# Kernel optimization log

Hardware: AMD Instinct MI355X
Metric: run time of the kernel (lower is better)

Reference implementation:

```python
import jax, jax.numpy as jnp
import numpy as np

H = 4        # num_heads
D = 16       # d_hid (per-head dim)
INF = 1e9


def setup_inputs() -> dict:
    key = jax.random.key(0)
    ks = jax.random.split(key, 8)
    T, R, DT, DZ = 4, 384, 64, 128
    t = jax.random.normal(ks[0], (T, R, R, DT), dtype=jnp.float32)
    z = jax.random.normal(ks[1], (R, R, DZ), dtype=jnp.float32)
    template_mask = jnp.ones((T,), dtype=jnp.float32)
    wq = jax.random.normal(ks[2], (DZ, H * D), dtype=jnp.float32) * 0.08
    wk = jax.random.normal(ks[3], (DT, H * D), dtype=jnp.float32) * 0.12
    wv = jax.random.normal(ks[4], (DT, H * D), dtype=jnp.float32) * 0.12
    wo = jax.random.normal(ks[5], (H * D, DZ), dtype=jnp.float32) * 0.12
    bo = jnp.zeros((DZ,), dtype=jnp.float32)
    return {"t": t, "z": z, "template_mask": template_mask,
            "wq": wq, "wk": wk, "wv": wv, "wo": wo, "bo": bo}


def reference(t, z, template_mask, wq, wk, wv, wo, bo):
    # t: [T, R, R, d_t], z: [R, R, d_z], template_mask: [T]
    R = z.shape[0]
    scale = 1.0 / np.sqrt(float(D))
    # gen_attn_mask: 0 where mask > 0, -inf where masked out
    bias = jnp.where(template_mask > 0.0, 0.0, -INF)          # [T]
    # permute_final_dims(t, (1,2,0,3)): template axis becomes kv length
    tp = jnp.transpose(t, (1, 2, 0, 3))                        # [R, R, T, d_t]
    # q_len is 1 (z.unsqueeze(-2)); fold it away
    q = (z @ wq).reshape(R, R, H, D) * scale                   # [R, R, H, D]
    k = (tp @ wk).reshape(R, R, -1, H, D)                      # [R, R, T, H, D]
    v = (tp @ wv).reshape(R, R, -1, H, D)                      # [R, R, T, H, D]
    logits = jnp.einsum('xyhd,xythd->xyht', q, k) + bias       # [R, R, H, T]
    a = jax.nn.softmax(logits, axis=-1)
    o = jnp.einsum('xyht,xythd->xyhd', a, v).reshape(R, R, H * D)
    return o @ wo + bo                                         # [R, R, d_z]
```

## Files before the change

kernel.cpp:

```cpp
#include <hip/hip_runtime.h>


typedef __bf16 bf16x8 __attribute__((ext_vector_type(8)));
typedef float f32x4 __attribute__((ext_vector_type(4)));
typedef unsigned int u32x4 __attribute__((ext_vector_type(4)));
typedef unsigned int u32x2 __attribute__((ext_vector_type(2)));

#define MFMA16(A, B, C) __builtin_amdgcn_mfma_f32_16x16x32_bf16((A), (B), (C), 0, 0, 0)

#define BARRIER_LGKM()                                      \
  do {                                                      \
    asm volatile("s_waitcnt lgkmcnt(0)" ::: "memory");      \
    __builtin_amdgcn_sched_barrier(0);                      \
    __builtin_amdgcn_s_barrier();                           \
    __builtin_amdgcn_sched_barrier(0);                      \
    asm volatile("" ::: "memory");                          \
  } while (0)

__device__ __forceinline__ unsigned int cvtpk(float lo, float hi) {
  unsigned int r;
  asm("v_cvt_pk_bf16_f32 %0, %1, %2" : "=v"(r) : "v"(lo), "v"(hi));
  return r;
}

__device__ __forceinline__ bf16x8 pack8(float4 a, float4 b) {
  u32x4 u;
  u.x = cvtpk(a.x, a.y);
  u.y = cvtpk(a.z, a.w);
  u.z = cvtpk(b.x, b.y);
  u.w = cvtpk(b.z, b.w);
  return __builtin_bit_cast(bf16x8, u);
}

__device__ __forceinline__ bf16x8 ldsA(const char* smem, int baseByte, int row,
                                       int colElem, int strideElem) {
  int off = baseByte + (((row * strideElem + colElem) * 2) ^ ((row & 7) << 4));
  return __builtin_bit_cast(bf16x8, *(const u32x4*)(smem + off));
}

__device__ __forceinline__ bf16x8 ldsT(const char* TB, int tt, int px, int kElem) {
  int off = ((((tt * 64 + px) << 7) + (kElem << 1))) ^ ((px & 7) << 4);
  return __builtin_bit_cast(bf16x8, *(const u32x4*)(TB + off));
}

__device__ __forceinline__ void stage_w(char* smem, int off, float v, int r, int j) {
  unsigned int u = __float_as_uint(v);
  *(unsigned short*)(smem + off + ((j * 2) ^ ((r & 7) << 4))) =
      (unsigned short)((u + 0x7fffu + ((u >> 16) & 1u)) >> 16);
}

__global__ __launch_bounds__(256, 2)
void q_kernel(const float* __restrict__ z_, const float* __restrict__ wq_,
              u32x2* __restrict__ q_) {
  extern __shared__ char smem[];
  for (int i = threadIdx.x; i < 8192; i += 256) {
    int r = i >> 7, cc = i & 127;
    stage_w(smem, 0, wq_[cc * 64 + r] * 0.25f, r, i);
  }
  __syncthreads();
  const int lane = threadIdx.x & 63;
  const int wid = threadIdx.x >> 6;
  const int c = lane & 15, g = lane >> 4;
  const f32x4 vz = {0.f, 0.f, 0.f, 0.f};
  for (int tile = blockIdx.x * 4 + wid; tile < 9216; tile += 4608) {
    const int p = tile * 16 + c;
    const float4* zp = (const float4*)(z_ + (size_t)p * 128 + g * 8);
    float4 zraw[8];
#pragma unroll
    for (int s = 0; s < 4; ++s) {
      zraw[2 * s] = zp[s * 8];
      zraw[2 * s + 1] = zp[s * 8 + 1];
    }
    f32x4 qacc[4] = {vz, vz, vz, vz};
#pragma unroll
    for (int s = 0; s < 4; ++s) {
      bf16x8 zb = pack8(zraw[2 * s], zraw[2 * s + 1]);
#pragma unroll
      for (int h = 0; h < 4; ++h)
        qacc[h] = MFMA16(ldsA(smem, 0, h * 16 + c, s * 32 + g * 8, 128), zb, qacc[h]);
    }
#pragma unroll
    for (int h = 0; h < 4; ++h) {
      u32x2 w;
      w.x = cvtpk(qacc[h][0], qacc[h][1]);
      w.y = cvtpk(qacc[h][2], qacc[h][3]);
      q_[(size_t)(tile * 4 + h) * 64 + lane] = w;
    }
  }
}

__global__ __launch_bounds__(512, 1)
void tpa_b_kernel(const float* __restrict__ t_, const u32x2* __restrict__ q_,
                  const float* __restrict__ mask_,
                  const float* __restrict__ wk_, const float* __restrict__ wv_,
                  const float* __restrict__ wo_, const float* __restrict__ bo_,
                  float* __restrict__ out_) {
  extern __shared__ char smem[];
  char* TB = smem + 32768;

  for (int i = threadIdx.x; i < 16384; i += 512) {
    if (i < 4096) {
      int r = i >> 6, cc = i & 63;
      stage_w(smem, 0, wk_[cc * 64 + r], r, i);
    } else if (i < 8192) {
      int j = i - 4096, r = j >> 6, cc = j & 63;
      stage_w(smem, 8192, wv_[cc * 64 + r], r, j);
    } else {
      int j = i - 8192, r = j >> 6, cc = j & 63;
      stage_w(smem, 16384, wo_[cc * 128 + r], r, j);
    }
  }
  __syncthreads();

  const int tid = threadIdx.x;
  const int lane = tid & 63, wid = tid >> 6;
  const int c = lane & 15, g = lane >> 4;
  const int q4 = wid & 3;
  const int hp = wid >> 2;
  const int px = q4 * 16 + c;
  char* Olds = smem + 65536 + q4 * 2048;

  const float b0 = mask_[0] > 0.f ? 0.f : -1e9f;
  const float b1 = mask_[1] > 0.f ? 0.f : -1e9f;
  const float b2 = mask_[2] > 0.f ? 0.f : -1e9f;
  const float b3 = mask_[3] > 0.f ? 0.f : -1e9f;

  float4 bov[4];
#pragma unroll
  for (int m = 0; m < 4; ++m) bov[m] = *(const float4*)(bo_ + hp * 64 + m * 16 + g * 4);

  const int spx = tid >> 3;
  const int schunk = tid & 7;
  const f32x4 vz = {0.f, 0.f, 0.f, 0.f};

  float4 ra[8];
  u32x2 qcur[2], qnext[2];

  auto issue_step = [&](int step, u32x2* qw) {
    const float* base = t_ + ((size_t)step * 64 + spx) * 64 + schunk * 8;
#pragma unroll
    for (int tt = 0; tt < 4; ++tt) {
      const float* p4 = base + (size_t)tt * 9437184;
      ra[tt * 2] = *(const float4*)(p4);
      ra[tt * 2 + 1] = *(const float4*)(p4 + 4);
    }
    const int stile = step * 4 + q4;
#pragma unroll
    for (int h = 0; h < 2; ++h)
      qw[h] = q_[(size_t)(stile * 4 + hp * 2 + h) * 64 + lane];
  };

  issue_step(blockIdx.x, qcur);

  for (int k = 0; k < 9; ++k) {
    const int step = blockIdx.x + k * 256;

#pragma unroll
    for (int tt = 0; tt < 4; ++tt) {
      bf16x8 w = pack8(ra[tt * 2], ra[tt * 2 + 1]);
      int off = ((((tt * 64 + spx) << 7) + (schunk << 4))) ^ ((spx & 7) << 4);
      *(u32x4*)(TB + off) = __builtin_bit_cast(u32x4, w);
    }
    if (k < 8) issue_step(step + 256, qnext);
    BARRIER_LGKM();

    f32x4 qacc[2];
#pragma unroll
    for (int h = 0; h < 2; ++h) {
      qacc[h][0] = __uint_as_float(qcur[h].x << 16);
      qacc[h][1] = __uint_as_float(qcur[h].x & 0xffff0000u);
      qacc[h][2] = __uint_as_float(qcur[h].y << 16);
      qacc[h][3] = __uint_as_float(qcur[h].y & 0xffff0000u);
    }
    f32x4 oacc[2] = {vz, vz};
    float ssum[2] = {0.f, 0.f};
#pragma unroll
    for (int tt = 0; tt < 4; ++tt) {
      bf16x8 tb0 = ldsT(TB, tt, px, g * 8);
      bf16x8 tb1 = ldsT(TB, tt, px, 32 + g * 8);
      const float bt = (tt == 0) ? b0 : (tt == 1) ? b1 : (tt == 2) ? b2 : b3;
#pragma unroll
      for (int h = 0; h < 2; ++h) {
        const int row = (hp * 2 + h) * 16 + c;
        f32x4 kacc = MFMA16(ldsA(smem, 0, row, g * 8, 64), tb0, vz);
        kacc = MFMA16(ldsA(smem, 0, row, 32 + g * 8, 64), tb1, kacc);
        f32x4 vacc = MFMA16(ldsA(smem, 8192, row, g * 8, 64), tb0, vz);
        vacc = MFMA16(ldsA(smem, 8192, row, 32 + g * 8, 64), tb1, vacc);
        float d = qacc[h][0] * kacc[0] + qacc[h][1] * kacc[1] +
                  qacc[h][2] * kacc[2] + qacc[h][3] * kacc[3];
        d += __shfl_xor(d, 16);
        d += __shfl_xor(d, 32);
        float e = __expf(d + bt);
        ssum[h] += e;
        oacc[h] += e * vacc;
      }
    }

#pragma unroll
    for (int h = 0; h < 2; ++h) {
      float inv = 1.0f / ssum[h];
      f32x4 o = oacc[h] * inv;
      u32x2 w;
      w.x = cvtpk(o[0], o[1]);
      w.y = cvtpk(o[2], o[3]);
      int off = (c * 128 + (hp * 2 + h) * 32 + g * 8) ^ ((c & 7) << 4);
      *(u32x2*)(Olds + off) = w;
    }
    BARRIER_LGKM();

    f32x4 outacc[4] = {vz, vz, vz, vz};
#pragma unroll
    for (int s = 0; s < 2; ++s) {
      int off = (c * 128 + s * 64 + g * 16) ^ ((c & 7) << 4);
      bf16x8 ob = __builtin_bit_cast(bf16x8, *(const u32x4*)(Olds + off));
#pragma unroll
      for (int m = 0; m < 4; ++m)
        outacc[m] = MFMA16(ldsA(smem, 16384, hp * 64 + m * 16 + c, s * 32 + g * 8, 64),
                           ob, outacc[m]);
    }
    float* op = out_ + ((size_t)step * 64 + px) * 128 + hp * 64;
#pragma unroll
    for (int m = 0; m < 4; ++m) {
      float4 st;
      st.x = outacc[m][0] + bov[m].x;
      st.y = outacc[m][1] + bov[m].y;
      st.z = outacc[m][2] + bov[m].z;
      st.w = outacc[m][3] + bov[m].w;
      *(float4*)(op + m * 16 + g * 4) = st;
    }
    if (k < 8) {
      qcur[0] = qnext[0];
      qcur[1] = qnext[1];
    }
  }
}

__global__ __launch_bounds__(256, 2)
void tpa_fused(const float* __restrict__ t_, const float* __restrict__ z_,
               const float* __restrict__ mask_,
               const float* __restrict__ wq_, const float* __restrict__ wk_,
               const float* __restrict__ wv_, const float* __restrict__ wo_,
               const float* __restrict__ bo_, float* __restrict__ out_) {
  extern __shared__ char smem[];
  for (int i = threadIdx.x; i < 24576; i += 256) {
    if (i < 8192) {
      int r = i >> 7;
      stage_w(smem, 0, wq_[(i & 127) * 64 + r] * 0.25f, r, i);
    } else if (i < 12288) {
      int j = i - 8192, r = j >> 6;
      stage_w(smem, 16384, wk_[(j & 63) * 64 + r], r, j);
    } else if (i < 16384) {
      int j = i - 12288, r = j >> 6;
      stage_w(smem, 24576, wv_[(j & 63) * 64 + r], r, j);
    } else {
      int j = i - 16384, r = j >> 6;
      stage_w(smem, 32768, wo_[(j & 63) * 128 + r], r, j);
    }
  }
  __syncthreads();
  const int lane = threadIdx.x & 63;
  const int wid = threadIdx.x >> 6;
  const int c = lane & 15, g = lane >> 4;
  const float b0 = mask_[0] > 0.f ? 0.f : -1e9f;
  const float b1 = mask_[1] > 0.f ? 0.f : -1e9f;
  const float b2 = mask_[2] > 0.f ? 0.f : -1e9f;
  const float b3 = mask_[3] > 0.f ? 0.f : -1e9f;
  char* Olds = smem + 49152 + wid * 2048;
  const f32x4 vz = {0.f, 0.f, 0.f, 0.f};
  for (int tile = blockIdx.x * 4 + wid; tile < 9216; tile += 2048) {
    const int p = tile * 16 + c;
    const float4* zp = (const float4*)(z_ + (size_t)p * 128 + g * 8);
    const float* tp = t_ + (size_t)p * 64 + g * 8;
    f32x4 qacc[4] = {vz, vz, vz, vz};
#pragma unroll
    for (int s = 0; s < 4; ++s) {
      bf16x8 zb = pack8(zp[s * 8], zp[s * 8 + 1]);
#pragma unroll
      for (int h = 0; h < 4; ++h)
        qacc[h] = MFMA16(ldsA(smem, 0, h * 16 + c, s * 32 + g * 8, 128), zb, qacc[h]);
    }
    f32x4 oacc[4] = {vz, vz, vz, vz};
    float ssum[4] = {0.f, 0.f, 0.f, 0.f};
#pragma unroll
    for (int tt = 0; tt < 4; ++tt) {
      const float* tq = tp + (size_t)tt * 9437184;
      bf16x8 tb0 = pack8(*(const float4*)(tq), *(const float4*)(tq + 4));
      bf16x8 tb1 = pack8(*(const float4*)(tq + 32), *(const float4*)(tq + 36));
      f32x4 kacc[4], vacc[4];
#pragma unroll
      for (int h = 0; h < 4; ++h) {
        kacc[h] = MFMA16(ldsA(smem, 16384, h * 16 + c, g * 8, 64), tb0, vz);
        kacc[h] = MFMA16(ldsA(smem, 16384, h * 16 + c, 32 + g * 8, 64), tb1, kacc[h]);
        vacc[h] = MFMA16(ldsA(smem, 24576, h * 16 + c, g * 8, 64), tb0, vz);
        vacc[h] = MFMA16(ldsA(smem, 24576, h * 16 + c, 32 + g * 8, 64), tb1, vacc[h]);
      }
      const float bt = (tt == 0) ? b0 : (tt == 1) ? b1 : (tt == 2) ? b2 : b3;
#pragma unroll
      for (int h = 0; h < 4; ++h) {
        float d = qacc[h][0] * kacc[h][0] + qacc[h][1] * kacc[h][1] +
                  qacc[h][2] * kacc[h][2] + qacc[h][3] * kacc[h][3];
        d += __shfl_xor(d, 16);
        d += __shfl_xor(d, 32);
        float e = __expf(d + bt);
        ssum[h] += e;
        oacc[h] += e * vacc[h];
      }
    }
#pragma unroll
    for (int h = 0; h < 4; ++h) {
      float inv = 1.0f / ssum[h];
      f32x4 o = oacc[h] * inv;
      u32x2 w;
      w.x = cvtpk(o[0], o[1]);
      w.y = cvtpk(o[2], o[3]);
      int off = (c * 128 + h * 32 + g * 8) ^ ((c & 7) << 4);
      *(u32x2*)(Olds + off) = w;
    }
    asm volatile("s_waitcnt lgkmcnt(0)" ::: "memory");
    f32x4 outacc[8] = {vz, vz, vz, vz, vz, vz, vz, vz};
#pragma unroll
    for (int s = 0; s < 2; ++s) {
      int off = (c * 128 + s * 64 + g * 16) ^ ((c & 7) << 4);
      bf16x8 ob = __builtin_bit_cast(bf16x8, *(const u32x4*)(Olds + off));
#pragma unroll
      for (int m = 0; m < 8; ++m)
        outacc[m] = MFMA16(ldsA(smem, 32768, m * 16 + c, s * 32 + g * 8, 64), ob, outacc[m]);
    }
    float* op = out_ + (size_t)p * 128;
    const float4* bop = (const float4*)bo_;
#pragma unroll
    for (int m = 0; m < 8; ++m) {
      float4 bv = bop[m * 4 + g];
      float4 st;
      st.x = outacc[m][0] + bv.x;
      st.y = outacc[m][1] + bv.y;
      st.z = outacc[m][2] + bv.z;
      st.w = outacc[m][3] + bv.w;
      *(float4*)(op + m * 16 + g * 4) = st;
    }
    asm volatile("" ::: "memory");
  }
}

extern "C" void kernel_launch(void* const* d_in, const int* in_sizes, int n_in,
                              void* d_out, int out_size, void* d_ws, size_t ws_size,
                              hipStream_t stream) {
  const float* t = (const float*)d_in[0];
  const float* z = (const float*)d_in[1];
  const float* mk = (const float*)d_in[2];
  const float* wq = (const float*)d_in[3];
  const float* wk = (const float*)d_in[4];
  const float* wv = (const float*)d_in[5];
  const float* wo = (const float*)d_in[6];
  const float* bo = (const float*)d_in[7];
  float* out = (float*)d_out;
  (void)in_sizes; (void)n_in; (void)out_size;

  const size_t qbytes = (size_t)9216 * 4 * 64 * 8;
  if (ws_size >= qbytes) {
    u32x2* qws = (u32x2*)d_ws;
    hipLaunchKernelGGL(q_kernel, dim3(1152), dim3(256), 16384, stream, z, wq, qws);
    hipLaunchKernelGGL(tpa_b_kernel, dim3(256), dim3(512), 73728, stream,
                       t, qws, mk, wk, wv, wo, bo, out);
  } else {
    hipLaunchKernelGGL(tpa_fused, dim3(512), dim3(256), 57344, stream,
                       t, z, mk, wq, wk, wv, wo, bo, out);
  }
}
```

Before: 91.64 us.

## Stream template tiles via direct global-to-LDS loads with double buffering

Replaces the register-staged fp32-to-bf16 conversion of the template tile with global_load_lds DMA into a double-buffered fp32 LDS region. The conversion to bf16 now happens when each wave reads the tile from LDS. It also hoists the Wk/Wv/Wo MFMA fragments into registers once per block, so they are no longer reloaded from LDS every iteration. The costs are a much larger LDS footprint (about 136 KB), more VGPR pressure, and a partial vmcnt wait that has to be counted correctly for the outstanding stores and loads.

```diff
diff --git a/kernel.cpp b/kernel.cpp
--- a/kernel.cpp
+++ b/kernel.cpp
@@ -17,6 +17,15 @@
     asm volatile("" ::: "memory");                          \
   } while (0)
 
+#define BARRIER_VM4()                                               \
+  do {                                                              \
+    asm volatile("s_waitcnt vmcnt(4) lgkmcnt(0)" ::: "memory");     \
+    __builtin_amdgcn_sched_barrier(0);                              \
+    __builtin_amdgcn_s_barrier();                                   \
+    __builtin_amdgcn_sched_barrier(0);                              \
+    asm volatile("" ::: "memory");                                  \
+  } while (0)
+
 __device__ __forceinline__ unsigned int cvtpk(float lo, float hi) {
   unsigned int r;
   asm("v_cvt_pk_bf16_f32 %0, %1, %2" : "=v"(r) : "v"(lo), "v"(hi));
@@ -32,15 +41,23 @@
   return __builtin_bit_cast(bf16x8, u);
 }
 
+__device__ __forceinline__ void gl_lds16(const float* g, char* l) {
+  __builtin_amdgcn_global_load_lds(
+      (const __attribute__((address_space(1))) unsigned int*)g,
+      (__attribute__((address_space(3))) unsigned int*)l, 16, 0, 0);
+}
+
 __device__ __forceinline__ bf16x8 ldsA(const char* smem, int baseByte, int row,
                                        int colElem, int strideElem) {
   int off = baseByte + (((row * strideElem + colElem) * 2) ^ ((row & 7) << 4));
   return __builtin_bit_cast(bf16x8, *(const u32x4*)(smem + off));
 }
 
-__device__ __forceinline__ bf16x8 ldsT(const char* TB, int tt, int px, int kElem) {
-  int off = ((((tt * 64 + px) << 7) + (kElem << 1))) ^ ((px & 7) << 4);
-  return __builtin_bit_cast(bf16x8, *(const u32x4*)(TB + off));
+__device__ __forceinline__ bf16x8 ldsT32(const char* TBcur, int tt, int pxl, int gr) {
+  const char* base = TBcur + tt * 16384 + pxl * 256;
+  float4 a = *(const float4*)(base + (((gr) ^ (pxl & 7)) << 4));
+  float4 b = *(const float4*)(base + (((gr + 1) ^ (pxl & 7)) << 4));
+  return pack8(a, b);
 }
 
 __device__ __forceinline__ void stage_w(char* smem, int off, float v, int r, int j) {
@@ -96,7 +113,7 @@
                   const float* __restrict__ wo_, const float* __restrict__ bo_,
                   float* __restrict__ out_) {
   extern __shared__ char smem[];
-  char* TB = smem + 32768;
+  char* TB = smem;
 
   for (int i = threadIdx.x; i < 16384; i += 512) {
     if (i < 4096) {
@@ -118,7 +135,22 @@
   const int q4 = wid & 3;
   const int hp = wid >> 2;
   const int px = q4 * 16 + c;
-  char* Olds = smem + 65536 + q4 * 2048;
+  char* Olds = smem + 131072 + q4 * 2048;
+
+  bf16x8 wkf[2][2], wvf[2][2], wof[2][4];
+#pragma unroll
+  for (int h = 0; h < 2; ++h)
+#pragma unroll
+    for (int s = 0; s < 2; ++s) {
+      wkf[h][s] = ldsA(smem, 0, (hp * 2 + h) * 16 + c, s * 32 + g * 8, 64);
+      wvf[h][s] = ldsA(smem, 8192, (hp * 2 + h) * 16 + c, s * 32 + g * 8, 64);
+    }
+#pragma unroll
+  for (int s = 0; s < 2; ++s)
+#pragma unroll
+    for (int m = 0; m < 4; ++m)
+      wof[s][m] = ldsA(smem, 16384, hp * 64 + m * 16 + c, s * 32 + g * 8, 64);
+  __syncthreads();
 
   const float b0 = mask_[0] > 0.f ? 0.f : -1e9f;
   const float b1 = mask_[1] > 0.f ? 0.f : -1e9f;
@@ -129,40 +161,47 @@
 #pragma unroll
   for (int m = 0; m < 4; ++m) bov[m] = *(const float4*)(bo_ + hp * 64 + m * 16 + g * 4);
 
-  const int spx = tid >> 3;
-  const int schunk = tid & 7;
   const f32x4 vz = {0.f, 0.f, 0.f, 0.f};
-
-  float4 ra[8];
   u32x2 qcur[2], qnext[2];
 
-  auto issue_step = [&](int step, u32x2* qw) {
-    const float* base = t_ + ((size_t)step * 64 + spx) * 64 + schunk * 8;
-#pragma unroll
-    for (int tt = 0; tt < 4; ++tt) {
-      const float* p4 = base + (size_t)tt * 9437184;
-      ra[tt * 2] = *(const float4*)(p4);
-      ra[tt * 2 + 1] = *(const float4*)(p4 + 4);
-    }
+  const int row_local = lane >> 4;
+  const int gran = lane & 15;
+
+  auto issue_t = [&](int step, char* TBdst) {
+#pragma unroll
+    for (int j = 0; j < 8; ++j) {
+      const int cw = wid * 8 + j;
+      const int tt = cw >> 4, cr = cw & 15;
+      char* ldst = TBdst + tt * 16384 + cr * 1024;
+      const int pxs = cr * 4 + row_local;
+      const int sg = gran ^ (pxs & 7);
+      const float* gsrc =
+          t_ + (size_t)tt * 9437184 + ((size_t)step * 64 + pxs) * 64 + sg * 4;
+      gl_lds16(gsrc, ldst);
+    }
+  };
+  auto issue_q = [&](int step, u32x2* qw) {
     const int stile = step * 4 + q4;
 #pragma unroll
     for (int h = 0; h < 2; ++h)
       qw[h] = q_[(size_t)(stile * 4 + hp * 2 + h) * 64 + lane];
   };
 
-  issue_step(blockIdx.x, qcur);
+  issue_t(blockIdx.x, TB);
+  issue_q(blockIdx.x, qcur);
+  asm volatile("s_waitcnt vmcnt(0)" ::: "memory");
+  __builtin_amdgcn_sched_barrier(0);
+  __builtin_amdgcn_s_barrier();
+  __builtin_amdgcn_sched_barrier(0);
 
   for (int k = 0; k < 9; ++k) {
     const int step = blockIdx.x + k * 256;
-
-#pragma unroll
-    for (int tt = 0; tt < 4; ++tt) {
-      bf16x8 w = pack8(ra[tt * 2], ra[tt * 2 + 1]);
-      int off = ((((tt * 64 + spx) << 7) + (schunk << 4))) ^ ((spx & 7) << 4);
-      *(u32x4*)(TB + off) = __builtin_bit_cast(u32x4, w);
-    }
-    if (k < 8) issue_step(step + 256, qnext);
-    BARRIER_LGKM();
+    char* TBcur = TB + ((k & 1) << 16);
+
+    if (k < 8) {
+      issue_t(step + 256, TB + (((k + 1) & 1) << 16));
+      issue_q(step + 256, qnext);
+    }
 
     f32x4 qacc[2];
 #pragma unroll
@@ -176,16 +215,15 @@
     float ssum[2] = {0.f, 0.f};
 #pragma unroll
     for (int tt = 0; tt < 4; ++tt) {
-      bf16x8 tb0 = ldsT(TB, tt, px, g * 8);
-      bf16x8 tb1 = ldsT(TB, tt, px, 32 + g * 8);
+      bf16x8 tb0 = ldsT32(TBcur, tt, px, g * 2);
+      bf16x8 tb1 = ldsT32(TBcur, tt, px, 8 + g * 2);
       const float bt = (tt == 0) ? b0 : (tt == 1) ? b1 : (tt == 2) ? b2 : b3;
 #pragma unroll
       for (int h = 0; h < 2; ++h) {
-        const int row = (hp * 2 + h) * 16 + c;
-        f32x4 kacc = MFMA16(ldsA(smem, 0, row, g * 8, 64), tb0, vz);
-        kacc = MFMA16(ldsA(smem, 0, row, 32 + g * 8, 64), tb1, kacc);
-        f32x4 vacc = MFMA16(ldsA(smem, 8192, row, g * 8, 64), tb0, vz);
-        vacc = MFMA16(ldsA(smem, 8192, row, 32 + g * 8, 64), tb1, vacc);
+        f32x4 kacc = MFMA16(wkf[h][0], tb0, vz);
+        kacc = MFMA16(wkf[h][1], tb1, kacc);
+        f32x4 vacc = MFMA16(wvf[h][0], tb0, vz);
+        vacc = MFMA16(wvf[h][1], tb1, vacc);
         float d = qacc[h][0] * kacc[0] + qacc[h][1] * kacc[1] +
                   qacc[h][2] * kacc[2] + qacc[h][3] * kacc[3];
         d += __shfl_xor(d, 16);
@@ -215,8 +253,7 @@
       bf16x8 ob = __builtin_bit_cast(bf16x8, *(const u32x4*)(Olds + off));
 #pragma unroll
       for (int m = 0; m < 4; ++m)
-        outacc[m] = MFMA16(ldsA(smem, 16384, hp * 64 + m * 16 + c, s * 32 + g * 8, 64),
-                           ob, outacc[m]);
+        outacc[m] = MFMA16(wof[s][m], ob, outacc[m]);
     }
     float* op = out_ + ((size_t)step * 64 + px) * 128 + hp * 64;
 #pragma unroll
@@ -228,7 +265,9 @@
       st.w = outacc[m][3] + bov[m].w;
       *(float4*)(op + m * 16 + g * 4) = st;
     }
+
     if (k < 8) {
+      BARRIER_VM4();
       qcur[0] = qnext[0];
       qcur[1] = qnext[1];
     }
@@ -360,7 +399,7 @@
   if (ws_size >= qbytes) {
     u32x2* qws = (u32x2*)d_ws;
     hipLaunchKernelGGL(q_kernel, dim3(1152), dim3(256), 16384, stream, z, wq, qws);
-    hipLaunchKernelGGL(tpa_b_kernel, dim3(256), dim3(512), 73728, stream,
+    hipLaunchKernelGGL(tpa_b_kernel, dim3(256), dim3(512), 139264, stream,
                        t, qws, mk, wk, wv, wo, bo, out);
   } else {
     hipLaunchKernelGGL(tpa_fused, dim3(512), dim3(256), 57344, stream,
```

Result: slower. 96.02 us (+4.8%).
